# Kernel tuning notes

Measured on AMD Instinct MI355X. Metric: run time of the kernel, lower is better.

The kernel has to match this reference:

```python
import jax, jax.numpy as jnp
import numpy as np
from jax import lax

NMS_THRESH = 0.7
PRE_NMS_TOPK = 1000
POST_NMS_TOPK = 256
MIN_SIZE = 0.0


def setup_inputs() -> dict:
    key = jax.random.key(0)
    ks = jax.random.split(key, 4)
    N, C, Hf, Wf, P = 2, 128, 256, 256, 9
    x = jax.random.normal(ks[0], (N, C, Hf, Wf), jnp.float32)
    # small weight scales keep exp(offsets*stride) in a sane range (offsets head is zero-init in torch)
    W_conv = jax.random.normal(ks[1], (C, C, 3, 3), jnp.float32) * 0.05
    b_conv = jnp.zeros((C,), jnp.float32)
    W_off = jax.random.normal(ks[2], (2 * P, C), jnp.float32) * 0.01
    b_off = jnp.zeros((2 * P,), jnp.float32)
    W_log = jax.random.normal(ks[3], (1, C), jnp.float32) * 0.05
    b_log = jnp.zeros((1,), jnp.float32)
    return {"x": x, "W_conv": W_conv, "b_conv": b_conv, "W_off": W_off,
            "b_off": b_off, "W_log": W_log, "b_log": b_log,
            "image_h": 2048, "image_w": 2048}


def _forward_dense(x, W_conv, b_conv, W_off, b_off, W_log, b_log, image_h, image_w):
    N, C, Hf, Wf = x.shape
    t = lax.conv_general_dilated(x, W_conv, (1, 1), ((1, 1), (1, 1)),
                                 dimension_numbers=("NCHW", "OIHW", "NCHW"))
    t = jax.nn.relu(t + b_conv[None, :, None, None])
    logits = jnp.einsum("nchw,oc->nohw", t, W_log) + b_log[None, :, None, None]  # (N,1,Hf,Wf)
    off = jnp.einsum("nchw,oc->nohw", t, W_off) + b_off[None, :, None, None]      # (N,18,Hf,Wf)
    scale = image_w / Wf  # rescale() asserts scale_x == scale_y
    off = jnp.exp(off * scale) - 1.0
    # offsets2coordinates -- faithful to the torch code, including the H/W linspace
    # swap (ys spans image W over Hf points, xs spans image H over Wf points);
    # benign for square images.
    ys_lin = jnp.linspace(0.0, image_w - 1.0, Hf)
    xs_lin = jnp.linspace(0.0, image_h - 1.0, Wf)
    ys = jnp.broadcast_to(ys_lin[:, None], (Hf, Wf))
    xs = jnp.broadcast_to(xs_lin[None, :], (Hf, Wf))
    coords = off.reshape(N, 9, 2, Hf, Wf) + jnp.stack([xs, ys], 0)[None, None]
    cx = jnp.clip(coords[:, :, 0], 0.0, image_w - 1.0)  # clamp(0, W-1)
    cy = jnp.clip(coords[:, :, 1], 0.0, image_h - 1.0)  # clamp(0, H-1)
    # predict_proposals: min/max over the 9 points -> [N, Hf*Wf, 4]
    boxes = jnp.stack([cx.min(1), cy.min(1), cx.max(1), cy.max(1)], -1).reshape(N, Hf * Wf, 4)
    scores = logits.reshape(N, Hf * Wf)
    return scores, boxes


def _iou_matrix(b):
    x1, y1, x2, y2 = b[:, 0], b[:, 1], b[:, 2], b[:, 3]
    area = (x2 - x1) * (y2 - y1)
    iw = jnp.clip(jnp.minimum(x2[:, None], x2[None, :]) - jnp.maximum(x1[:, None], x1[None, :]), 0.0)
    ih = jnp.clip(jnp.minimum(y2[:, None], y2[None, :]) - jnp.maximum(y1[:, None], y1[None, :]), 0.0)
    inter = iw * ih
    return inter / (area[:, None] + area[None, :] - inter + 1e-9)


def _nms_one_image(scores, boxes):
    # pre-NMS topk (scores already returned sorted descending by top_k)
    sc, idx = lax.top_k(scores, PRE_NMS_TOPK)
    b = boxes[idx]
    w = b[:, 2] - b[:, 0]
    h = b[:, 3] - b[:, 1]
    valid = (w >= MIN_SIZE) & (h >= MIN_SIZE)
    sc = jnp.where(valid, sc, -jnp.inf)
    iou = _iou_matrix(b)
    ar = jnp.arange(PRE_NMS_TOPK)

    def body(i, sup):
        alive = (~sup[i]) & valid[i]
        return sup | ((iou[i] > NMS_THRESH) & (ar > i) & alive)

    sup = lax.fori_loop(0, PRE_NMS_TOPK, body, jnp.zeros((PRE_NMS_TOPK,), bool))
    keep_sc = jnp.where(sup, -jnp.inf, sc)
    final_sc, fidx = lax.top_k(keep_sc, POST_NMS_TOPK)
    return b[fidx], final_sc


def reference(x, W_conv, b_conv, W_off, b_off, W_log, b_log, image_h, image_w):
    scores, boxes = _forward_dense(x, W_conv, b_conv, W_off, b_off, W_log, b_log, image_h, image_w)
    out = jnp.concatenate([scores[..., None], boxes], axis=-1)  # (N, Hf*Wf, 5)
    kept_boxes, kept_scores = jax.vmap(_nms_one_image)(scores, boxes)
    return out, kept_boxes, kept_scores
```

## Files before the change

### kernel.cpp

```cpp
#include <hip/hip_runtime.h>
#include <stdint.h>

typedef unsigned int u32;
typedef unsigned long long u64;
typedef __attribute__((ext_vector_type(8))) short short8;
typedef __attribute__((ext_vector_type(16))) float f32x16;

#define DEVI __device__ __forceinline__

constexpr int PRE_K = 1000;
constexpr int CAP = 8192;

constexpr size_t WF_OFF    = 0;
constexpr size_t HIST_OFF  = 884736;
constexpr size_t CNT_OFF   = 917504;
constexpr size_t CUT_OFF   = 917568;
constexpr size_t CAND_OFF  = 917632;
constexpr size_t TB_OFF    = 1048704;
constexpr size_t SCS_OFF   = 1080704;
constexpr size_t MASK_OFF  = 1088768;
constexpr size_t SCARR_OFF = 1350912;
constexpr size_t WS_NEED   = 1875200;

constexpr size_t KB_OFF = 655360;
constexpr size_t KS_OFF = 657408;

DEVI u32 fkey(float f) {
  u32 u = __float_as_uint(f);
  return (u & 0x80000000u) ? ~u : (u | 0x80000000u);
}

DEVI u64 shfl64(u64 v, int src) {
  int lo = __shfl((int)(u32)v, src, 64);
  int hi = __shfl((int)(u32)(v >> 32), src, 64);
  return ((u64)(u32)hi << 32) | (u64)(u32)lo;
}

DEVI u32 rne16(u32 u) { return (u + 0x7FFFu + ((u >> 16) & 1u)) >> 16; }

__global__ void wsplitk(const float* __restrict__ wc, float* __restrict__ wf) {
  int j = blockIdx.x * 256 + threadIdx.x;
  if (j >= 18432) return;
  int co = j / 144;
  int koct = j % 144;
  short8 h8, m8, l8;
#pragma unroll
  for (int jj = 0; jj < 8; ++jj) {
    int kk = koct * 8 + jj;
    int tap = kk >> 7, ci = kk & 127;
    float v = wc[(co * 128 + ci) * 9 + tap];
    u32 u0 = __float_as_uint(v);
    u32 hb = rne16(u0);
    float r1 = v - __uint_as_float(hb << 16);
    u32 u1 = __float_as_uint(r1);
    u32 mb = rne16(u1);
    float r2 = r1 - __uint_as_float(mb << 16);
    u32 lb = rne16(__float_as_uint(r2));
    h8[jj] = (short)hb; m8[jj] = (short)mb; l8[jj] = (short)lb;
  }
  int slot = ((koct & 1) << 5) + (co & 31);
  int kg = koct >> 1;
  int cblk = co >> 5;
  char* base = (char*)wf;
  *(short8*)(base + ((size_t)((0 * 4 + cblk) * 72 + kg) * 64 + slot) * 16) = h8;
  *(short8*)(base + ((size_t)((1 * 4 + cblk) * 72 + kg) * 64 + slot) * 16) = m8;
  *(short8*)(base + ((size_t)((2 * 4 + cblk) * 72 + kg) * 64 + slot) * 16) = l8;
}

__global__ __launch_bounds__(256, 2) void convk(
    const float* __restrict__ x, const float* __restrict__ wf,
    const float* __restrict__ bconv,
    const float* __restrict__ woff, const float* __restrict__ boff,
    const float* __restrict__ wlog, const float* __restrict__ blog,
    const int* __restrict__ ihp, const int* __restrict__ iwp,
    float* __restrict__ out, u32* __restrict__ hist, float* __restrict__ scarr)
{
  __shared__ union {
    float halo[10][18][36];
    float tch[2][32][132];
  } sm;

  const int tid = threadIdx.x;
  const int l = tid & 63, wv = tid >> 6;
  const int mhalf = wv >> 1, nhalf = wv & 1;
  const int lm = l & 31, lg = l >> 5;
  const int bx = blockIdx.x, by = blockIdx.y, n = blockIdx.z;

  f32x16 acc[2][2];
#pragma unroll
  for (int mi = 0; mi < 2; ++mi)
#pragma unroll
    for (int ni = 0; ni < 2; ++ni)
#pragma unroll
      for (int q = 0; q < 16; ++q) acc[mi][ni][q] = 0.f;

#pragma unroll 1
  for (int cb = 0; cb < 4; ++cb) {
    __syncthreads();
    for (int e = tid; e < 5760; e += 256) {
      int ci = e / 180, rem = e % 180;
      int hh = rem / 18, ww = rem % 18;
      int gh = by * 8 + hh - 1, gw = bx * 16 + ww - 1;
      float v = 0.f;
      if ((unsigned)gh < 256u && (unsigned)gw < 256u)
        v = x[(((size_t)n * 128 + cb * 32 + ci) * 256 + gh) * 256 + gw];
      sm.halo[hh][ww][ci] = v;
    }
    __syncthreads();

#pragma unroll 1
    for (int tap = 0; tap < 9; ++tap) {
      int dy = tap / 3 - 1, dx = tap % 3 - 1;
      short8 Af[3][2][2];
#pragma unroll
      for (int mi = 0; mi < 2; ++mi) {
        int hh = mhalf * 4 + mi * 2 + (lm >> 4) + dy + 1;
        int ww = (lm & 15) + dx + 1;
#pragma unroll
        for (int ks = 0; ks < 2; ++ks) {
          const float* ap = &sm.halo[hh][ww][ks * 16 + lg * 8];
          float4 va = *(const float4*)ap;
          float4 vb = *(const float4*)(ap + 4);
          float fv[8] = {va.x, va.y, va.z, va.w, vb.x, vb.y, vb.z, vb.w};
          short8 ah, am, al;
#pragma unroll
          for (int jj = 0; jj < 8; ++jj) {
            u32 u0 = __float_as_uint(fv[jj]);
            u32 hb = rne16(u0);
            float r1 = fv[jj] - __uint_as_float(hb << 16);
            u32 u1 = __float_as_uint(r1);
            u32 mb = rne16(u1);
            float r2 = r1 - __uint_as_float(mb << 16);
            u32 lb = rne16(__float_as_uint(r2));
            ah[jj] = (short)hb; am[jj] = (short)mb; al[jj] = (short)lb;
          }
          Af[0][mi][ks] = ah; Af[1][mi][ks] = am; Af[2][mi][ks] = al;
        }
      }
      const char* wfb = (const char*)wf;
#pragma unroll
      for (int sb = 0; sb < 3; ++sb) {
        short8 Bf[2][2];
#pragma unroll
        for (int ni = 0; ni < 2; ++ni)
#pragma unroll
          for (int ks = 0; ks < 2; ++ks) {
            int fid = (sb * 4 + nhalf * 2 + ni) * 72 + tap * 8 + cb * 2 + ks;
            Bf[ni][ks] = *(const short8*)(wfb + ((size_t)fid * 64 + l) * 16);
          }
#pragma unroll
        for (int sa = 0; sa < 3 - sb; ++sa)
#pragma unroll
          for (int mi = 0; mi < 2; ++mi)
#pragma unroll
            for (int ni = 0; ni < 2; ++ni)
#pragma unroll
              for (int ks = 0; ks < 2; ++ks)
                acc[mi][ni] = __builtin_amdgcn_mfma_f32_32x32x16_bf16(
                    Af[sa][mi][ks], Bf[ni][ks], acc[mi][ni], 0, 0, 0);
      }
    }
  }

  __syncthreads();
  const int ihv = ihp[0], iwv = iwp[0];
  float bcv[2];
  bcv[0] = bconv[nhalf * 64 + lm];
  bcv[1] = bconv[nhalf * 64 + 32 + lm];
  const int cq = l >> 4;
  const int pxl = (nhalf << 4) + (l & 15);
  const float scale = (float)iwv / 256.0f;

#pragma unroll
  for (int r = 0; r < 2; ++r) {
    if (r) __syncthreads();
#pragma unroll
    for (int ni = 0; ni < 2; ++ni)
#pragma unroll
      for (int rg = 0; rg < 16; ++rg) {
        int row = (rg & 3) + ((rg >> 2) << 3) + ((l >> 5) << 2);
        sm.tch[mhalf][row][(nhalf << 6) + (ni << 5) + lm] =
            fmaxf(acc[r][ni][rg] + bcv[ni], 0.f);
      }
    __syncthreads();

    float tv[32];
#pragma unroll
    for (int i = 0; i < 8; ++i) {
      float4 t4 = *(const float4*)&sm.tch[mhalf][pxl][(cq << 5) + (i << 2)];
      tv[i * 4 + 0] = t4.x; tv[i * 4 + 1] = t4.y;
      tv[i * 4 + 2] = t4.z; tv[i * 4 + 3] = t4.w;
    }
    float s19[19];
#pragma unroll
    for (int o = 0; o < 19; ++o) {
      const float* wh = (o < 18) ? (woff + o * 128) : wlog;
      const float4* w4 = (const float4*)(wh + (cq << 5));
      float a0 = 0.f;
#pragma unroll
      for (int i = 0; i < 8; ++i) {
        float4 wv4 = w4[i];
        a0 = fmaf(tv[i * 4 + 0], wv4.x, a0);
        a0 = fmaf(tv[i * 4 + 1], wv4.y, a0);
        a0 = fmaf(tv[i * 4 + 2], wv4.z, a0);
        a0 = fmaf(tv[i * 4 + 3], wv4.w, a0);
      }
      s19[o] = a0;
    }
#pragma unroll
    for (int o = 0; o < 19; ++o) {
      s19[o] += __shfl_xor(s19[o], 16, 64);
      s19[o] += __shfl_xor(s19[o], 32, 64);
    }
    if (cq == 0) {
      int bpx = (mhalf << 6) + (r << 5) + pxl;
      int ph = bpx >> 4, pw = bpx & 15;
      int gh = by * 8 + ph, gw = bx * 16 + pw;
      float sc = s19[18] + blog[0];
      float xv = (float)((double)gw * ((double)(ihv - 1) / 255.0));
      float yv = (float)((double)gh * ((double)(iwv - 1) / 255.0));
      float mnx = __builtin_inff(), mny = __builtin_inff();
      float mxx = -__builtin_inff(), mxy = -__builtin_inff();
#pragma unroll
      for (int p = 0; p < 9; ++p) {
        float ox = expf((s19[2 * p] + boff[2 * p]) * scale) - 1.f + xv;
        float oy = expf((s19[2 * p + 1] + boff[2 * p + 1]) * scale) - 1.f + yv;
        float cx2 = fminf(fmaxf(ox, 0.f), (float)(iwv - 1));
        float cy2 = fminf(fmaxf(oy, 0.f), (float)(ihv - 1));
        mnx = fminf(mnx, cx2); mxx = fmaxf(mxx, cx2);
        mny = fminf(mny, cy2); mxy = fmaxf(mxy, cy2);
      }
      size_t pix = (size_t)n * 65536 + (size_t)gh * 256 + gw;
      float* rec = out + pix * 5;
      rec[0] = sc; rec[1] = mnx; rec[2] = mny; rec[3] = mxx; rec[4] = mxy;
      if (scarr) scarr[pix] = sc;
      atomicAdd(&hist[n * 4096 + (fkey(sc) >> 20)], 1u);
    }
  }
}

__global__ __launch_bounds__(256) void cutoffk(const u32* __restrict__ hist, u32* __restrict__ cut) {
  int n = blockIdx.x;
  const u32* h = hist + n * 4096;
  __shared__ u32 pre[256];
  int t = threadIdx.x;
  u32 s0 = 0;
  for (int k = 0; k < 16; ++k) s0 += h[4095 - (t * 16 + k)];
  pre[t] = s0;
  __syncthreads();
  for (int off = 1; off < 256; off <<= 1) {
    u32 add = (t >= off) ? pre[t - off] : 0u;
    __syncthreads();
    pre[t] += add;
    __syncthreads();
  }
  u32 incl = pre[t];
  u32 excl = incl - s0;
  if (incl >= (u32)PRE_K && excl < (u32)PRE_K) {
    u32 cum = excl;
    for (int k = 0; k < 16; ++k) {
      int b = 4095 - (t * 16 + k);
      cum += h[b];
      if (cum >= (u32)PRE_K) { cut[n] = ((u32)b) << 20; break; }
    }
  }
}

__global__ void collectk(const float* __restrict__ out, const float* __restrict__ scarr,
                         const u32* __restrict__ cut,
                         u32* __restrict__ cnt, u64* __restrict__ cand) {
  int e = blockIdx.x * 256 + threadIdx.x;
  int n = e >> 16;
  u32 pix = e & 65535;
  float sc = scarr ? scarr[e] : out[((size_t)n * 65536 + pix) * 5];
  u32 key = fkey(sc);
  if (key >= cut[n]) {
    u32 pos = atomicAdd(&cnt[n], 1u);
    if (pos < (u32)CAP)
      cand[(size_t)n * CAP + pos] = ((u64)key << 32) | (u64)(0xFFFFFFFFu - pix);
  }
}

__global__ __launch_bounds__(1024) void ranksel(const u64* __restrict__ cand, const u32* __restrict__ cnt,
                                                const float* __restrict__ out,
                                                float* __restrict__ tb, float* __restrict__ scs) {
  int n = blockIdx.x;
  int t = threadIdx.x;
  __shared__ u64 d[CAP];
  u32 m = cnt[n]; if (m > (u32)CAP) m = CAP;
  for (int i = t; i < (int)m; i += 1024) d[i] = cand[(size_t)n * CAP + i];
  __syncthreads();
  for (int i = t; i < (int)m; i += 1024) {
    u64 ki = d[i];
    u32 r = 0;
    for (u32 j = 0; j < m; ++j) r += (d[j] > ki) ? 1u : 0u;
    if (r < (u32)PRE_K) {
      u32 pix = 0xFFFFFFFFu - (u32)(ki & 0xFFFFFFFFull);
      const float* rec = out + ((size_t)n * 65536 + pix) * 5;
      float sc = rec[0];
      float b0 = rec[1], b1 = rec[2], b2 = rec[3], b3 = rec[4];
      bool valid = ((b2 - b0) >= 0.f) && ((b3 - b1) >= 0.f);
      scs[n * PRE_K + r] = valid ? sc : -__builtin_inff();
      float* tbp = tb + ((size_t)n * PRE_K + r) * 4;
      tbp[0] = b0; tbp[1] = b1; tbp[2] = b2; tbp[3] = b3;
    }
  }
}

__global__ __launch_bounds__(1024) void maskk(const float* __restrict__ tb, u64* __restrict__ maskw) {
  int c = blockIdx.x;
  int n = blockIdx.y;
  int t = threadIdx.x;
  __shared__ float bx[PRE_K][4];
  for (int e = t; e < PRE_K * 4; e += 1024) ((float*)bx)[e] = tb[(size_t)n * PRE_K * 4 + e];
  __syncthreads();
  u64 accm = 0;
  if (t < PRE_K) {
    float x1 = bx[t][0], y1 = bx[t][1], x2 = bx[t][2], y2 = bx[t][3];
    float ai = (x2 - x1) * (y2 - y1);
    int j0 = max(t + 1, c * 64), j1 = min(PRE_K, c * 64 + 64);
    for (int j = j0; j < j1; ++j) {
      float u1 = bx[j][0], v1 = bx[j][1], u2 = bx[j][2], v2 = bx[j][3];
      float aj = (u2 - u1) * (v2 - v1);
      float iw = fminf(x2, u2) - fmaxf(x1, u1); iw = fmaxf(iw, 0.f);
      float ih = fminf(y2, v2) - fmaxf(y1, v1); ih = fmaxf(ih, 0.f);
      float inter = iw * ih;
      float iou = inter / (ai + aj - inter + 1e-9f);
      if (iou > 0.7f) accm |= (1ull << (j & 63));
    }
  }
  maskw[((size_t)n * 1024 + t) * 16 + c] = accm;
}

__global__ __launch_bounds__(64) void finalk(const u64* __restrict__ maskw,
                                             const float* __restrict__ scs,
                                             const float* __restrict__ tb,
                                             float* __restrict__ out) {
  int n = blockIdx.x;
  int lane = threadIdx.x;
  __shared__ float lsc[1024];
  __shared__ unsigned short ordA[1024];
  __shared__ unsigned short ordB[1024];
  for (int e = lane; e < 1024; e += 64)
    lsc[e] = (e < PRE_K) ? scs[n * PRE_K + e] : -__builtin_inff();
  __syncthreads();

  u64 sup = 0;
#pragma unroll
  for (int c = 0; c < 16; ++c) {
    u64 b = __ballot(!(lsc[c * 64 + lane] > -__builtin_inff()));
    if (lane == c) sup = b;
  }

  const u64* gm = maskw + (size_t)n * 1024 * 16;
  u64 pre[16];
#pragma unroll
  for (int d = 0; d < 16; ++d)
    pre[d] = (lane < 16) ? gm[d * 16 + lane] : 0ull;

  for (int i0 = 0; i0 < 1024; i0 += 16) {
#pragma unroll
    for (int d = 0; d < 16; ++d) {
      int i = i0 + d;
      u64 mi = pre[d];
      int nx = i + 16;
      pre[d] = (nx < 1024 && lane < 16) ? gm[(size_t)nx * 16 + lane] : 0ull;
      int w = i >> 6;
      u64 sw = shfl64(sup, w);
      bool supbit = (sw >> (i & 63)) & 1ull;
      if (!supbit) sup |= mi;
    }
  }

  u64 ltm = (1ull << lane) - 1ull;
  u32 baseA = 0, baseB = 0;
  for (int c = 0; c < 16; ++c) {
    int i = c * 64 + lane;
    u64 sw = shfl64(sup, c);
    bool bit = (sw >> lane) & 1ull;
    bool vi = i < PRE_K;
    bool sf = vi && !bit && (lsc[vi ? i : 0] > -__builtin_inff());
    u64 mA = __ballot(sf);
    u64 mB = __ballot(vi && !sf);
    if (sf) ordA[baseA + __popcll(mA & ltm)] = (unsigned short)i;
    else if (vi) ordB[baseB + __popcll(mB & ltm)] = (unsigned short)i;
    baseA += (u32)__popcll(mA);
    baseB += (u32)__popcll(mB);
  }
  __syncthreads();

  for (int r = 0; r < 4; ++r) {
    int k = r * 64 + lane;
    int fi; float v;
    if (k < (int)baseA) { fi = ordA[k]; v = lsc[fi]; }
    else { fi = ordB[k - baseA]; v = -__builtin_inff(); }
    const float* bp = tb + ((size_t)n * PRE_K + fi) * 4;
    float* kb = out + KB_OFF + ((size_t)n * 256 + k) * 4;
    kb[0] = bp[0]; kb[1] = bp[1]; kb[2] = bp[2]; kb[3] = bp[3];
    out[KS_OFF + (size_t)n * 256 + k] = v;
  }
}

extern "C" void kernel_launch(void* const* d_in, const int* in_sizes, int n_in,
                              void* d_out, int out_size, void* d_ws, size_t ws_size,
                              hipStream_t stream) {
  const float* x     = (const float*)d_in[0];
  const float* wc    = (const float*)d_in[1];
  const float* bconv = (const float*)d_in[2];
  const float* woff  = (const float*)d_in[3];
  const float* boff  = (const float*)d_in[4];
  const float* wlog  = (const float*)d_in[5];
  const float* blog  = (const float*)d_in[6];
  const int* ihp     = (const int*)d_in[7];
  const int* iwp     = (const int*)d_in[8];
  float* out = (float*)d_out;
  char* ws = (char*)d_ws;

  float* wf   = (float*)(ws + WF_OFF);
  u32* hist   = (u32*)(ws + HIST_OFF);
  u32* cnt    = (u32*)(ws + CNT_OFF);
  u32* cut    = (u32*)(ws + CUT_OFF);
  u64* cand   = (u64*)(ws + CAND_OFF);
  float* tb   = (float*)(ws + TB_OFF);
  float* scs  = (float*)(ws + SCS_OFF);
  u64* maskw  = (u64*)(ws + MASK_OFF);
  float* scarr = (ws_size >= WS_NEED) ? (float*)(ws + SCARR_OFF) : nullptr;

  hipMemsetAsync(ws + HIST_OFF, 0, (CAND_OFF - HIST_OFF), stream);
  hipLaunchKernelGGL(wsplitk, dim3(72), dim3(256), 0, stream, wc, wf);
  hipLaunchKernelGGL(convk, dim3(16, 32, 2), dim3(256), 0, stream,
                     x, wf, bconv, woff, boff, wlog, blog, ihp, iwp, out, hist, scarr);
  hipLaunchKernelGGL(cutoffk, dim3(2), dim3(256), 0, stream, hist, cut);
  hipLaunchKernelGGL(collectk, dim3(512), dim3(256), 0, stream, out, scarr, cut, cnt, cand);
  hipLaunchKernelGGL(ranksel, dim3(2), dim3(1024), 0, stream, cand, cnt, out, tb, scs);
  hipLaunchKernelGGL(maskk, dim3(16, 2), dim3(1024), 0, stream, tb, maskw);
  hipLaunchKernelGGL(finalk, dim3(2), dim3(64), 0, stream, maskw, scs, tb, out);
}
```

Measured before the change: 629.9 us.

## Pre-split input halo to bf16 planes in LDS and shrink conv LDS footprint

```diff
diff --git a/kernel.cpp b/kernel.cpp
--- a/kernel.cpp
+++ b/kernel.cpp
@@ -3,6 +3,7 @@
 
 typedef unsigned int u32;
 typedef unsigned long long u64;
+typedef __attribute__((ext_vector_type(4))) short short4v;
 typedef __attribute__((ext_vector_type(8))) short short8;
 typedef __attribute__((ext_vector_type(16))) float f32x16;
 
@@ -38,8 +39,11 @@
 
 DEVI u32 rne16(u32 u) { return (u + 0x7FFFu + ((u >> 16) & 1u)) >> 16; }
 
-__global__ void wsplitk(const float* __restrict__ wc, float* __restrict__ wf) {
+__global__ void wsplitk(const float* __restrict__ wc, float* __restrict__ wf,
+                        u32* __restrict__ hist, u32* __restrict__ cnt) {
   int j = blockIdx.x * 256 + threadIdx.x;
+  if (j < 8192) hist[j] = 0;
+  if (j < 2) cnt[j] = 0;
   if (j >= 18432) return;
   int co = j / 144;
   int koct = j % 144;
@@ -52,8 +56,7 @@
     u32 u0 = __float_as_uint(v);
     u32 hb = rne16(u0);
     float r1 = v - __uint_as_float(hb << 16);
-    u32 u1 = __float_as_uint(r1);
-    u32 mb = rne16(u1);
+    u32 mb = rne16(__float_as_uint(r1));
     float r2 = r1 - __uint_as_float(mb << 16);
     u32 lb = rne16(__float_as_uint(r2));
     h8[jj] = (short)hb; m8[jj] = (short)mb; l8[jj] = (short)lb;
@@ -76,8 +79,8 @@
     float* __restrict__ out, u32* __restrict__ hist, float* __restrict__ scarr)
 {
   __shared__ union {
-    float halo[10][18][36];
-    float tch[2][32][132];
+    unsigned short pl[3 * 3600];
+    float tq[32][132];
   } sm;
 
   const int tid = threadIdx.x;
@@ -94,70 +97,65 @@
 #pragma unroll
       for (int q = 0; q < 16; ++q) acc[mi][ni][q] = 0.f;
 
+  const char* wfb = (const char*)wf;
+
 #pragma unroll 1
-  for (int cb = 0; cb < 4; ++cb) {
+  for (int cc = 0; cc < 8; ++cc) {
     __syncthreads();
-    for (int e = tid; e < 5760; e += 256) {
+    const float* xbase = x + ((size_t)n * 128 + cc * 16) * 65536;
+    for (int e = tid; e < 2880; e += 256) {
       int ci = e / 180, rem = e % 180;
       int hh = rem / 18, ww = rem % 18;
       int gh = by * 8 + hh - 1, gw = bx * 16 + ww - 1;
       float v = 0.f;
       if ((unsigned)gh < 256u && (unsigned)gw < 256u)
-        v = x[(((size_t)n * 128 + cb * 32 + ci) * 256 + gh) * 256 + gw];
-      sm.halo[hh][ww][ci] = v;
+        v = xbase[(size_t)ci * 65536 + gh * 256 + gw];
+      u32 u0 = __float_as_uint(v);
+      u32 hb = rne16(u0);
+      float r1 = v - __uint_as_float(hb << 16);
+      u32 mb = rne16(__float_as_uint(r1));
+      float r2 = r1 - __uint_as_float(mb << 16);
+      u32 lb = rne16(__float_as_uint(r2));
+      int idx = (hh * 18 + ww) * 20 + ci;
+      sm.pl[idx] = (unsigned short)hb;
+      sm.pl[idx + 3600] = (unsigned short)mb;
+      sm.pl[idx + 7200] = (unsigned short)lb;
     }
     __syncthreads();
 
 #pragma unroll 1
     for (int tap = 0; tap < 9; ++tap) {
       int dy = tap / 3 - 1, dx = tap % 3 - 1;
-      short8 Af[3][2][2];
+      short8 Af[3][2];
 #pragma unroll
       for (int mi = 0; mi < 2; ++mi) {
         int hh = mhalf * 4 + mi * 2 + (lm >> 4) + dy + 1;
         int ww = (lm & 15) + dx + 1;
-#pragma unroll
-        for (int ks = 0; ks < 2; ++ks) {
-          const float* ap = &sm.halo[hh][ww][ks * 16 + lg * 8];
-          float4 va = *(const float4*)ap;
-          float4 vb = *(const float4*)(ap + 4);
-          float fv[8] = {va.x, va.y, va.z, va.w, vb.x, vb.y, vb.z, vb.w};
-          short8 ah, am, al;
-#pragma unroll
-          for (int jj = 0; jj < 8; ++jj) {
-            u32 u0 = __float_as_uint(fv[jj]);
-            u32 hb = rne16(u0);
-            float r1 = fv[jj] - __uint_as_float(hb << 16);
-            u32 u1 = __float_as_uint(r1);
-            u32 mb = rne16(u1);
-            float r2 = r1 - __uint_as_float(mb << 16);
-            u32 lb = rne16(__float_as_uint(r2));
-            ah[jj] = (short)hb; am[jj] = (short)mb; al[jj] = (short)lb;
-          }
-          Af[0][mi][ks] = ah; Af[1][mi][ks] = am; Af[2][mi][ks] = al;
+        int base = (hh * 18 + ww) * 20 + lg * 8;
+#pragma unroll
+        for (int s = 0; s < 3; ++s) {
+          short4v a0 = *(const short4v*)&sm.pl[s * 3600 + base];
+          short4v a1 = *(const short4v*)&sm.pl[s * 3600 + base + 4];
+          short8 v8 = {a0[0], a0[1], a0[2], a0[3], a1[0], a1[1], a1[2], a1[3]};
+          Af[s][mi] = v8;
         }
       }
-      const char* wfb = (const char*)wf;
 #pragma unroll
       for (int sb = 0; sb < 3; ++sb) {
-        short8 Bf[2][2];
-#pragma unroll
-        for (int ni = 0; ni < 2; ++ni)
-#pragma unroll
-          for (int ks = 0; ks < 2; ++ks) {
-            int fid = (sb * 4 + nhalf * 2 + ni) * 72 + tap * 8 + cb * 2 + ks;
-            Bf[ni][ks] = *(const short8*)(wfb + ((size_t)fid * 64 + l) * 16);
-          }
+        short8 Bf[2];
+#pragma unroll
+        for (int ni = 0; ni < 2; ++ni) {
+          int fid = (sb * 4 + nhalf * 2 + ni) * 72 + tap * 8 + cc;
+          Bf[ni] = *(const short8*)(wfb + ((size_t)fid * 64 + l) * 16);
+        }
 #pragma unroll
         for (int sa = 0; sa < 3 - sb; ++sa)
 #pragma unroll
           for (int mi = 0; mi < 2; ++mi)
 #pragma unroll
             for (int ni = 0; ni < 2; ++ni)
-#pragma unroll
-              for (int ks = 0; ks < 2; ++ks)
-                acc[mi][ni] = __builtin_amdgcn_mfma_f32_32x32x16_bf16(
-                    Af[sa][mi][ks], Bf[ni][ks], acc[mi][ni], 0, 0, 0);
+              acc[mi][ni] = __builtin_amdgcn_mfma_f32_32x32x16_bf16(
+                  Af[sa][mi], Bf[ni], acc[mi][ni], 0, 0, 0);
       }
     }
   }
@@ -171,70 +169,76 @@
   const int pxl = (nhalf << 4) + (l & 15);
   const float scale = (float)iwv / 256.0f;
 
-#pragma unroll
-  for (int r = 0; r < 2; ++r) {
-    if (r) __syncthreads();
-#pragma unroll
-    for (int ni = 0; ni < 2; ++ni)
-#pragma unroll
-      for (int rg = 0; rg < 16; ++rg) {
-        int row = (rg & 3) + ((rg >> 2) << 3) + ((l >> 5) << 2);
-        sm.tch[mhalf][row][(nhalf << 6) + (ni << 5) + lm] =
-            fmaxf(acc[r][ni][rg] + bcv[ni], 0.f);
+#pragma unroll 1
+  for (int mh = 0; mh < 2; ++mh) {
+#pragma unroll 1
+    for (int r = 0; r < 2; ++r) {
+      if (mh || r) __syncthreads();
+      if (mhalf == mh) {
+#pragma unroll
+        for (int ni = 0; ni < 2; ++ni)
+#pragma unroll
+          for (int rg = 0; rg < 16; ++rg) {
+            int row = (rg & 3) + ((rg >> 2) << 3) + ((l >> 5) << 2);
+            sm.tq[row][(nhalf << 6) + (ni << 5) + lm] =
+                fmaxf((r ? acc[1][ni][rg] : acc[0][ni][rg]) + bcv[ni], 0.f);
+          }
       }
-    __syncthreads();
-
-    float tv[32];
-#pragma unroll
-    for (int i = 0; i < 8; ++i) {
-      float4 t4 = *(const float4*)&sm.tch[mhalf][pxl][(cq << 5) + (i << 2)];
-      tv[i * 4 + 0] = t4.x; tv[i * 4 + 1] = t4.y;
-      tv[i * 4 + 2] = t4.z; tv[i * 4 + 3] = t4.w;
-    }
-    float s19[19];
-#pragma unroll
-    for (int o = 0; o < 19; ++o) {
-      const float* wh = (o < 18) ? (woff + o * 128) : wlog;
-      const float4* w4 = (const float4*)(wh + (cq << 5));
-      float a0 = 0.f;
-#pragma unroll
-      for (int i = 0; i < 8; ++i) {
-        float4 wv4 = w4[i];
-        a0 = fmaf(tv[i * 4 + 0], wv4.x, a0);
-        a0 = fmaf(tv[i * 4 + 1], wv4.y, a0);
-        a0 = fmaf(tv[i * 4 + 2], wv4.z, a0);
-        a0 = fmaf(tv[i * 4 + 3], wv4.w, a0);
+      __syncthreads();
+      if (mhalf == mh) {
+        float tv[32];
+#pragma unroll
+        for (int i = 0; i < 8; ++i) {
+          float4 t4 = *(const float4*)&sm.tq[pxl][(cq << 5) + (i << 2)];
+          tv[i * 4 + 0] = t4.x; tv[i * 4 + 1] = t4.y;
+          tv[i * 4 + 2] = t4.z; tv[i * 4 + 3] = t4.w;
+        }
+        float s19[19];
+#pragma unroll
+        for (int o = 0; o < 19; ++o) {
+          const float* wh = (o < 18) ? (woff + o * 128) : wlog;
+          const float4* w4 = (const float4*)(wh + (cq << 5));
+          float a0 = 0.f;
+#pragma unroll
+          for (int i = 0; i < 8; ++i) {
+            float4 wv4 = w4[i];
+            a0 = fmaf(tv[i * 4 + 0], wv4.x, a0);
+            a0 = fmaf(tv[i * 4 + 1], wv4.y, a0);
+            a0 = fmaf(tv[i * 4 + 2], wv4.z, a0);
+            a0 = fmaf(tv[i * 4 + 3], wv4.w, a0);
+          }
+          s19[o] = a0;
+        }
+#pragma unroll
+        for (int o = 0; o < 19; ++o) {
+          s19[o] += __shfl_xor(s19[o], 16, 64);
+          s19[o] += __shfl_xor(s19[o], 32, 64);
+        }
+        if (cq == 0) {
+          int bpx = (mh << 6) + (r << 5) + pxl;
+          int ph = bpx >> 4, pw = bpx & 15;
+          int gh = by * 8 + ph, gw = bx * 16 + pw;
+          float sc = s19[18] + blog[0];
+          float xv = (float)((double)gw * ((double)(ihv - 1) / 255.0));
+          float yv = (float)((double)gh * ((double)(iwv - 1) / 255.0));
+          float mnx = __builtin_inff(), mny = __builtin_inff();
+          float mxx = -__builtin_inff(), mxy = -__builtin_inff();
+#pragma unroll
+          for (int p = 0; p < 9; ++p) {
+            float ox = expf((s19[2 * p] + boff[2 * p]) * scale) - 1.f + xv;
+            float oy = expf((s19[2 * p + 1] + boff[2 * p + 1]) * scale) - 1.f + yv;
+            float cx2 = fminf(fmaxf(ox, 0.f), (float)(iwv - 1));
+            float cy2 = fminf(fmaxf(oy, 0.f), (float)(ihv - 1));
+            mnx = fminf(mnx, cx2); mxx = fmaxf(mxx, cx2);
+            mny = fminf(mny, cy2); mxy = fmaxf(mxy, cy2);
+          }
+          size_t pix = (size_t)n * 65536 + (size_t)gh * 256 + gw;
+          float* rec = out + pix * 5;
+          rec[0] = sc; rec[1] = mnx; rec[2] = mny; rec[3] = mxx; rec[4] = mxy;
+          if (scarr) scarr[pix] = sc;
+          atomicAdd(&hist[n * 4096 + (fkey(sc) >> 20)], 1u);
+        }
       }
-      s19[o] = a0;
-    }
-#pragma unroll
-    for (int o = 0; o < 19; ++o) {
-      s19[o] += __shfl_xor(s19[o], 16, 64);
-      s19[o] += __shfl_xor(s19[o], 32, 64);
-    }
-    if (cq == 0) {
-      int bpx = (mhalf << 6) + (r << 5) + pxl;
-      int ph = bpx >> 4, pw = bpx & 15;
-      int gh = by * 8 + ph, gw = bx * 16 + pw;
-      float sc = s19[18] + blog[0];
-      float xv = (float)((double)gw * ((double)(ihv - 1) / 255.0));
-      float yv = (float)((double)gh * ((double)(iwv - 1) / 255.0));
-      float mnx = __builtin_inff(), mny = __builtin_inff();
-      float mxx = -__builtin_inff(), mxy = -__builtin_inff();
-#pragma unroll
-      for (int p = 0; p < 9; ++p) {
-        float ox = expf((s19[2 * p] + boff[2 * p]) * scale) - 1.f + xv;
-        float oy = expf((s19[2 * p + 1] + boff[2 * p + 1]) * scale) - 1.f + yv;
-        float cx2 = fminf(fmaxf(ox, 0.f), (float)(iwv - 1));
-        float cy2 = fminf(fmaxf(oy, 0.f), (float)(ihv - 1));
-        mnx = fminf(mnx, cx2); mxx = fmaxf(mxx, cx2);
-        mny = fminf(mny, cy2); mxy = fmaxf(mxy, cy2);
-      }
-      size_t pix = (size_t)n * 65536 + (size_t)gh * 256 + gw;
-      float* rec = out + pix * 5;
-      rec[0] = sc; rec[1] = mnx; rec[2] = mny; rec[3] = mxx; rec[4] = mxy;
-      if (scarr) scarr[pix] = sc;
-      atomicAdd(&hist[n * 4096 + (fkey(sc) >> 20)], 1u);
     }
   }
 }
@@ -416,18 +420,17 @@
   float* out = (float*)d_out;
   char* ws = (char*)d_ws;
 
-  float* wf   = (float*)(ws + WF_OFF);
-  u32* hist   = (u32*)(ws + HIST_OFF);
-  u32* cnt    = (u32*)(ws + CNT_OFF);
-  u32* cut    = (u32*)(ws + CUT_OFF);
-  u64* cand   = (u64*)(ws + CAND_OFF);
-  float* tb   = (float*)(ws + TB_OFF);
-  float* scs  = (float*)(ws + SCS_OFF);
-  u64* maskw  = (u64*)(ws + MASK_OFF);
+  float* wf    = (float*)(ws + WF_OFF);
+  u32* hist    = (u32*)(ws + HIST_OFF);
+  u32* cnt     = (u32*)(ws + CNT_OFF);
+  u32* cut     = (u32*)(ws + CUT_OFF);
+  u64* cand    = (u64*)(ws + CAND_OFF);
+  float* tb    = (float*)(ws + TB_OFF);
+  float* scs   = (float*)(ws + SCS_OFF);
+  u64* maskw   = (u64*)(ws + MASK_OFF);
   float* scarr = (ws_size >= WS_NEED) ? (float*)(ws + SCARR_OFF) : nullptr;
 
-  hipMemsetAsync(ws + HIST_OFF, 0, (CAND_OFF - HIST_OFF), stream);
-  hipLaunchKernelGGL(wsplitk, dim3(72), dim3(256), 0, stream, wc, wf);
+  hipLaunchKernelGGL(wsplitk, dim3(72), dim3(256), 0, stream, wc, wf, hist, cnt);
   hipLaunchKernelGGL(convk, dim3(16, 32, 2), dim3(256), 0, stream,
                      x, wf, bconv, woff, boff, wlog, blog, ihp, iwp, out, hist, scarr);
   hipLaunchKernelGGL(cutoffk, dim3(2), dim3(256), 0, stream, hist, cut);
```

New measurement: 654.8 us. 4.0% more time.
